# Performance work log

Measured on AMD Instinct MI355X. Metric: run time of the kernel, lower is better.

## Reference

```python
import jax, jax.numpy as jnp
import numpy as np

NUM_QUBITS = 12
ENC_COPIES = 1
ANSATZ_COPIES = 2
BATCH = 1024
NUM_THETAS = NUM_QUBITS * (ANSATZ_COPIES + 1) * 2  # 72

_H = jnp.asarray(np.array([[1.0, 1.0], [1.0, -1.0]], np.complex64) / np.sqrt(2.0))


def _apply_1q(state, U, q):
    # state: [B, 2, 2, ..., 2] (n qubit axes); apply 2x2 unitary U on qubit q
    s = jnp.moveaxis(state, 1 + q, -1)
    s = jnp.einsum('...j,ij->...i', s, U)
    return jnp.moveaxis(s, -1, 1 + q)


def _apply_zpow(state, t, q):
    # cirq Z**t = diag(1, e^{i*pi*t}); t is scalar or per-batch [B]
    n = state.ndim - 1
    phase = jnp.exp(1j * jnp.pi * t).astype(jnp.complex64)
    factor = jnp.stack([jnp.ones_like(phase), phase], axis=-1)
    if factor.ndim == 2:  # batched exponent -> broadcast over other qubit axes
        factor = factor.reshape((factor.shape[0],) + (1,) * (n - 1) + (2,))
    s = jnp.moveaxis(state, 1 + q, -1)
    return jnp.moveaxis(s * factor, -1, 1 + q)


def _ypow_unitary(t):
    # cirq Y**t up to global phase e^{i*pi*t/2} (irrelevant for Z expectations)
    a = 0.5 * jnp.pi * t
    c, s = jnp.cos(a), jnp.sin(a)
    return jnp.stack([jnp.stack([c, -s]), jnp.stack([s, c])]).astype(jnp.complex64)


def _apply_cnot(state, c, t):
    s = jnp.moveaxis(state, (1 + c, 1 + t), (-2, -1))
    s = jnp.stack([s[..., 0, :], s[..., 1, ::-1]], axis=-2)
    return jnp.moveaxis(s, (-2, -1), (1 + c, 1 + t))


def _encoding_block(state, x):
    # FirstOrderPauliZEncoding: per copy, per qubit: H then Z**x_q
    for _ in range(ENC_COPIES):
        for q in range(NUM_QUBITS):
            state = _apply_1q(state, _H, q)
            state = _apply_zpow(state, x[:, q], q)
    return state


def _ansatz_block(state, th, with_cnot):
    # EfficientSU2 layer: Y**th[q,0], Z**th[q,1] per qubit, then CNOT chain
    for q in range(NUM_QUBITS):
        state = _apply_1q(state, _ypow_unitary(th[q, 0]), q)
        state = _apply_zpow(state, th[q, 1], q)
    if with_cnot:
        for q in range(NUM_QUBITS - 1):
            state = _apply_cnot(state, q, q + 1)
    return state


_enc = jax.checkpoint(_encoding_block)
_ans_cnot = jax.checkpoint(lambda st, th: _ansatz_block(st, th, True))
_ans_last = jax.checkpoint(lambda st, th: _ansatz_block(st, th, False))


def _circuit(inputs, thetas):
    b = inputs.shape[0]
    state = jnp.zeros((b, 2 ** NUM_QUBITS), jnp.complex64).at[:, 0].set(1.0)
    state = state.reshape((b,) + (2,) * NUM_QUBITS)
    state = _enc(state, inputs)
    th = thetas.reshape(ANSATZ_COPIES + 1, NUM_QUBITS, 2)
    for l in range(ANSATZ_COPIES + 1):
        state = (_ans_cnot if l < ANSATZ_COPIES else _ans_last)(state, th[l])
    # readouts: <Z_q> for each qubit
    probs = state.real ** 2 + state.imag ** 2
    exps = []
    for q in range(NUM_QUBITS):
        axes = tuple(a for a in range(1, NUM_QUBITS + 1) if a != 1 + q)
        p = probs.sum(axis=axes)  # [B, 2]
        exps.append(p[:, 0] - p[:, 1])
    return jnp.stack(exps, axis=-1)  # [B, NUM_QUBITS]


def setup_inputs() -> dict:
    key = jax.random.key(0)
    k1, k2 = jax.random.split(key)
    inputs = jax.random.uniform(k1, (BATCH, NUM_QUBITS), jnp.float32)
    thetas = jax.random.uniform(k2, (NUM_THETAS,), jnp.float32, minval=-1.0, maxval=1.0)
    return {"inputs": inputs, "thetas": thetas}


def reference(inputs, thetas):
    return _circuit(inputs, thetas)
```

## Files before the change

kernel.cpp:

```cpp
#include <hip/hip_runtime.h>


#define PI_F 3.14159265358979323846f
#define NR 16

typedef __attribute__((ext_vector_type(2))) float v2f;
typedef __attribute__((ext_vector_type(4))) float v4f;

__device__ __forceinline__ v2f mkv(float x, float y) { v2f r; r.x = x; r.y = y; return r; }

__device__ __forceinline__ v2f cmul(v2f a, v2f b) {
    return a.x * b + a.y * mkv(-b.y, b.x);
}
__device__ __forceinline__ v2f cmulc(v2f a, v2f b) {
    return a.x * mkv(b.x, -b.y) + a.y * mkv(b.y, b.x);
}

template<int M>
__device__ __forceinline__ float lane_xor_f(float v) {
    if constexpr (M == 1) {
        return __int_as_float(__builtin_amdgcn_update_dpp(
            0, __float_as_int(v), 0xB1, 0xF, 0xF, false));
    } else if constexpr (M == 2) {
        return __int_as_float(__builtin_amdgcn_update_dpp(
            0, __float_as_int(v), 0x4E, 0xF, 0xF, false));
    } else if constexpr (M == 4) {
        return __int_as_float(__builtin_amdgcn_ds_swizzle(__float_as_int(v), 0x101F));
    } else if constexpr (M == 8) {
        return __int_as_float(__builtin_amdgcn_ds_swizzle(__float_as_int(v), 0x201F));
    } else if constexpr (M == 16) {
        return __int_as_float(__builtin_amdgcn_ds_swizzle(__float_as_int(v), 0x401F));
    } else {
        return __shfl_xor(v, 32, 64);
    }
}
template<int M>
__device__ __forceinline__ v2f lane_xor_v(v2f v) {
    return mkv(lane_xor_f<M>(v.x), lane_xor_f<M>(v.y));
}

template<int RB>
__device__ __forceinline__ void ypow_reg(v2f (&a)[NR], float c, float s) {
    #pragma unroll
    for (int r0 = 0; r0 < NR; ++r0) {
        if ((r0 >> RB) & 1) continue;
        const int r1 = r0 | (1 << RB);
        v2f a0 = a[r0], a1 = a[r1];
        a[r0] = c * a0 - s * a1;
        a[r1] = s * a0 + c * a1;
    }
}

template<int M>
__device__ __forceinline__ void ypow_lane(v2f (&a)[NR], int lane, float c, float s) {
    const float k1 = (lane & M) ? s : -s;
    #pragma unroll
    for (int r = 0; r < NR; ++r) {
        v2f p = lane_xor_v<M>(a[r]);
        a[r] = c * a[r] + k1 * p;
    }
}

__device__ __forceinline__ void ypowB(v2f (&a)[NR], const float* __restrict__ th) {
    { float s,c; __sincosf(0.5f*PI_F*th[16], &s,&c); ypow_reg<3>(a,c,s); }
    { float s,c; __sincosf(0.5f*PI_F*th[18], &s,&c); ypow_reg<2>(a,c,s); }
    { float s,c; __sincosf(0.5f*PI_F*th[20], &s,&c); ypow_reg<1>(a,c,s); }
    { float s,c; __sincosf(0.5f*PI_F*th[22], &s,&c); ypow_reg<0>(a,c,s); }
}

__device__ __forceinline__ void ypow_lanes(v2f (&a)[NR], int lane,
                                           const float* __restrict__ th) {
    { float s,c; __sincosf(0.5f*PI_F*th[4],  &s,&c); ypow_lane<32>(a,lane,c,s); }
    { float s,c; __sincosf(0.5f*PI_F*th[6],  &s,&c); ypow_lane<16>(a,lane,c,s); }
    { float s,c; __sincosf(0.5f*PI_F*th[8],  &s,&c); ypow_lane<8>(a,lane,c,s); }
    { float s,c; __sincosf(0.5f*PI_F*th[10], &s,&c); ypow_lane<4>(a,lane,c,s); }
    { float s,c; __sincosf(0.5f*PI_F*th[12], &s,&c); ypow_lane<2>(a,lane,c,s); }
    { float s,c; __sincosf(0.5f*PI_F*th[14], &s,&c); ypow_lane<1>(a,lane,c,s); }
}

__device__ __forceinline__ void exchange_BB(v2f (&a)[NR], char* bufc,
                                            int w, int lane, bool preSync,
                                            float c0, float s0, float c1, float s1) {
    if (preSync) __syncthreads();
    const int v_ = (w >> 1) & 1;
    const int u_ = v_ ^ (w & 1);
    const int s9 = ((lane >> 5) ^ u_) & 1;
    const int wbyte = (s9 << 14) | ((lane & 31) << 9) | (u_ << 4) | (v_ << 3);
    #pragma unroll
    for (int r = 0; r < NR; ++r) {
        const int byt = wbyte | (r << 5);
        const int key = (((byt >> 9) ^ (byt >> 12)) & 7) << 4;
        *(v2f*)(bufc + (byt ^ key)) = a[r];
    }
    __syncthreads();
    const float ky00 = (w & 2) ? s0 : c0;
    const float ky01 = (w & 2) ? c0 : -s0;
    const float ky10 = (w & 1) ? s1 : c1;
    const float ky11 = (w & 1) ? c1 : -s1;
    const float k00 = ky10*ky00, k01 = ky10*ky01, k10 = ky11*ky00, k11 = ky11*ky01;
    #pragma unroll
    for (int r = 0; r < NR; ++r) {
        const int ylow = (lane << 4) | r;
        const int t = ylow ^ (ylow >> 1);
        const int base = t << 5;
        const int key = (((base >> 9) ^ (base >> 12)) & 7) << 4;
        v4f p01 = *(const v4f*)(bufc + (base ^ key));
        v4f p23 = *(const v4f*)(bufc + ((base | 16) ^ key));
        a[r] = k00 * p01.xy + k01 * p01.zw + k10 * p23.xy + k11 * p23.zw;
        if ((r & 7) == 7) asm volatile("" ::: "memory");
    }
}

__device__ __forceinline__ void fused_z_B(v2f (&a)[NR], int w, int lane,
                                          const float* __restrict__ th) {
    float alpha = ((w & 2) ? th[1] : 0.0f) + ((w & 1) ? th[3] : 0.0f);
    #pragma unroll
    for (int k = 0; k < 6; ++k)
        alpha += ((lane >> k) & 1) ? th[2*(7-k)+1] : 0.0f;
    float zbs, zbc; __sincosf(PI_F * alpha, &zbs, &zbc);
    v2f zq[4];
    #pragma unroll
    for (int j = 0; j < 4; ++j) {
        float ss, cc; __sincosf(PI_F * th[2*(11-j)+1], &ss, &cc);
        zq[j] = mkv(cc, ss);
    }
    v2f cur = mkv(zbc, zbs);
    a[0] = cmul(a[0], cur);
    #pragma unroll
    for (int k = 1; k < NR; ++k) {
        const int bit = __builtin_ctz(k);
        const int g = k ^ (k >> 1);
        cur = ((g >> bit) & 1) ? cmul(cur, zq[bit]) : cmulc(cur, zq[bit]);
        a[g] = cmul(a[g], cur);
    }
}

__global__ __launch_bounds__(256) void vqc_kernel(
    const float* __restrict__ inputs,
    const float* __restrict__ thetas,
    float* __restrict__ out)
{
    __shared__ __align__(16) char bufc[32768];

    const int b = blockIdx.x;
    const int tid = threadIdx.x;
    const int w = tid >> 6;
    const int lane = tid & 63;
    const float* x = inputs + b * 12;

    v2f a[NR];

    float phb = 0.0f;
    #pragma unroll
    for (int k = 0; k < 6; ++k)
        phb += ((lane >> k) & 1) ? x[7 - k] : 0.0f;
    float cbs, cbc; __sincosf(PI_F * phb, &cbs, &cbc);
    v2f cisb = mkv(cbc, cbs);
    float e0s, e0c; __sincosf(PI_F * x[0], &e0s, &e0c);
    float e1s, e1c; __sincosf(PI_F * x[1], &e1s, &e1c);
    float sa, ca; __sincosf(0.5f * PI_F * thetas[0], &sa, &ca);
    float sb, cb; __sincosf(0.5f * PI_F * thetas[2], &sb, &cb);
    v2f F0 = (w & 2) ? mkv(sa + ca*e0c,  ca*e0s)
                     : mkv(ca - sa*e0c, -sa*e0s);
    v2f F1 = (w & 1) ? mkv(sb + cb*e1c,  cb*e1s)
                     : mkv(cb - sb*e1c, -sb*e1s);
    v2f g0 = cmul(cmul(F0, F1), cisb);
    g0 = g0 * 0.015625f;
    v2f zr[4];
    #pragma unroll
    for (int j = 0; j < 4; ++j) {
        float ss, cc; __sincosf(PI_F * x[11 - j], &ss, &cc);
        zr[j] = mkv(cc, ss);
    }
    {
        v2f cur = g0;
        a[0] = cur;
        #pragma unroll
        for (int k = 1; k < NR; ++k) {
            const int bit = __builtin_ctz(k);
            const int g = k ^ (k >> 1);
            cur = ((g >> bit) & 1) ? cmul(cur, zr[bit]) : cmulc(cur, zr[bit]);
            a[g] = cur;
        }
    }

    const float* th0 = thetas;
    const float* th1 = thetas + 24;
    const float* th2 = thetas + 48;

    ypowB(a, th0);
    ypow_lanes(a, lane, th0);
    fused_z_B(a, w, lane, th0);
    { float s0,c0,s1,c1;
      __sincosf(0.5f*PI_F*th1[0], &s0,&c0);
      __sincosf(0.5f*PI_F*th1[2], &s1,&c1);
      exchange_BB(a, bufc, w, lane, false, c0,s0,c1,s1); }

    ypowB(a, th1);
    ypow_lanes(a, lane, th1);
    fused_z_B(a, w, lane, th1);
    { float s0,c0,s1,c1;
      __sincosf(0.5f*PI_F*th2[0], &s0,&c0);
      __sincosf(0.5f*PI_F*th2[2], &s1,&c1);
      exchange_BB(a, bufc, w, lane, true, c0,s0,c1,s1); }

    ypowB(a, th2);
    ypow_lanes(a, lane, th2);

    float totalP = 0.0f;
    float D[4] = {0, 0, 0, 0};
    #pragma unroll
    for (int r = 0; r < NR; ++r) {
        const float p = a[r].x * a[r].x + a[r].y * a[r].y;
        totalP += p;
        #pragma unroll
        for (int j = 0; j < 4; ++j)
            D[j] += ((r >> j) & 1) ? -p : p;
    }
    float* redBuf = (float*)bufc;
    __syncthreads();
    #pragma unroll
    for (int q = 0; q < 12; ++q) {
        float v;
        if (q == 0)      v = (w & 2) ? -totalP : totalP;
        else if (q == 1) v = (w & 1) ? -totalP : totalP;
        else if (q <= 7) v = ((lane >> (7 - q)) & 1) ? -totalP : totalP;
        else             v = D[11 - q];
        v += lane_xor_f<32>(v);
        v += lane_xor_f<16>(v);
        v += lane_xor_f<8>(v);
        v += lane_xor_f<4>(v);
        v += lane_xor_f<2>(v);
        v += lane_xor_f<1>(v);
        if (lane == 0) redBuf[w * 12 + q] = v;
    }
    __syncthreads();
    if (tid < 12)
        out[b * 12 + tid] = redBuf[tid] + redBuf[12 + tid]
                          + redBuf[24 + tid] + redBuf[36 + tid];
}

extern "C" void kernel_launch(void* const* d_in, const int* in_sizes, int n_in,
                              void* d_out, int out_size, void* d_ws, size_t ws_size,
                              hipStream_t stream) {
    const float* inputs = (const float*)d_in[0];
    const float* thetas = (const float*)d_in[1];
    float* out = (float*)d_out;
    vqc_kernel<<<dim3(1024), dim3(256), 0, stream>>>(inputs, thetas, out);
}
```

Measured before the change: 81.94 us.

## Split state over 8 waves with 8 registers per thread and three-qubit exchange

Changes the state distribution from 4 waves x 16 register amplitudes to 8 waves x 8 registers per thread, launching 512 threads per block. The LDS exchange now mixes three wave-held qubits per pass instead of two, with a new swizzle layout, and the xor-16 lane swap switches from ds_swizzle to shfl. This halves per-thread register work and raises the number of active waves, at the cost of more LDS reads per exchange and more cross-wave reduction.

After: 86.27 us. 5.3% more time.

```diff
diff --git a/kernel.cpp b/kernel.cpp
--- a/kernel.cpp
+++ b/kernel.cpp
@@ -2,7 +2,7 @@
 
 
 #define PI_F 3.14159265358979323846f
-#define NR 16
+#define NR 8
 
 typedef __attribute__((ext_vector_type(2))) float v2f;
 typedef __attribute__((ext_vector_type(4))) float v4f;
@@ -29,7 +29,7 @@
     } else if constexpr (M == 8) {
         return __int_as_float(__builtin_amdgcn_ds_swizzle(__float_as_int(v), 0x201F));
     } else if constexpr (M == 16) {
-        return __int_as_float(__builtin_amdgcn_ds_swizzle(__float_as_int(v), 0x401F));
+        return __shfl_xor(v, 16, 64);
     } else {
         return __shfl_xor(v, 32, 64);
     }
@@ -61,8 +61,7 @@
     }
 }
 
-__device__ __forceinline__ void ypowB(v2f (&a)[NR], const float* __restrict__ th) {
-    { float s,c; __sincosf(0.5f*PI_F*th[16], &s,&c); ypow_reg<3>(a,c,s); }
+__device__ __forceinline__ void ypow_regs(v2f (&a)[NR], const float* __restrict__ th) {
     { float s,c; __sincosf(0.5f*PI_F*th[18], &s,&c); ypow_reg<2>(a,c,s); }
     { float s,c; __sincosf(0.5f*PI_F*th[20], &s,&c); ypow_reg<1>(a,c,s); }
     { float s,c; __sincosf(0.5f*PI_F*th[22], &s,&c); ypow_reg<0>(a,c,s); }
@@ -70,57 +69,73 @@
 
 __device__ __forceinline__ void ypow_lanes(v2f (&a)[NR], int lane,
                                            const float* __restrict__ th) {
-    { float s,c; __sincosf(0.5f*PI_F*th[4],  &s,&c); ypow_lane<32>(a,lane,c,s); }
-    { float s,c; __sincosf(0.5f*PI_F*th[6],  &s,&c); ypow_lane<16>(a,lane,c,s); }
-    { float s,c; __sincosf(0.5f*PI_F*th[8],  &s,&c); ypow_lane<8>(a,lane,c,s); }
-    { float s,c; __sincosf(0.5f*PI_F*th[10], &s,&c); ypow_lane<4>(a,lane,c,s); }
-    { float s,c; __sincosf(0.5f*PI_F*th[12], &s,&c); ypow_lane<2>(a,lane,c,s); }
-    { float s,c; __sincosf(0.5f*PI_F*th[14], &s,&c); ypow_lane<1>(a,lane,c,s); }
-}
-
-__device__ __forceinline__ void exchange_BB(v2f (&a)[NR], char* bufc,
-                                            int w, int lane, bool preSync,
-                                            float c0, float s0, float c1, float s1) {
+    { float s,c; __sincosf(0.5f*PI_F*th[6],  &s,&c); ypow_lane<32>(a,lane,c,s); }
+    { float s,c; __sincosf(0.5f*PI_F*th[8],  &s,&c); ypow_lane<16>(a,lane,c,s); }
+    { float s,c; __sincosf(0.5f*PI_F*th[10], &s,&c); ypow_lane<8>(a,lane,c,s); }
+    { float s,c; __sincosf(0.5f*PI_F*th[12], &s,&c); ypow_lane<4>(a,lane,c,s); }
+    { float s,c; __sincosf(0.5f*PI_F*th[14], &s,&c); ypow_lane<2>(a,lane,c,s); }
+    { float s,c; __sincosf(0.5f*PI_F*th[16], &s,&c); ypow_lane<1>(a,lane,c,s); }
+}
+
+__device__ __forceinline__ void exchange_C(v2f (&a)[NR], char* bufc,
+                                           int wv, int lane, bool preSync,
+                                           float c0, float s0, float c1, float s1,
+                                           float c2, float s2) {
     if (preSync) __syncthreads();
-    const int v_ = (w >> 1) & 1;
-    const int u_ = v_ ^ (w & 1);
-    const int s9 = ((lane >> 5) ^ u_) & 1;
-    const int wbyte = (s9 << 14) | ((lane & 31) << 9) | (u_ << 4) | (v_ << 3);
-    #pragma unroll
-    for (int r = 0; r < NR; ++r) {
-        const int byt = wbyte | (r << 5);
-        const int key = (((byt >> 9) ^ (byt >> 12)) & 7) << 4;
-        *(v2f*)(bufc + (byt ^ key)) = a[r];
+    const int z11 = (wv >> 2) & 1;
+    const int z10 = ((wv >> 1) ^ (wv >> 2)) & 1;
+    const int z9  = (wv ^ (wv >> 1) ^ (wv >> 2)) & 1;
+    const int m_w = (z9 << 2) | (z10 << 1) | z11;
+    int U6 = lane; U6 ^= U6 >> 1; U6 ^= U6 >> 2; U6 ^= U6 >> 4; U6 &= 63;
+    if (z9) U6 ^= 63;
+    const int kxW   = (U6 >> 1) & 3;
+    const int key6W = (U6 >> 3) & 1;
+    const int wbase = (U6 << 9) | ((((m_w >> 1) & 3) ^ kxW) << 4) | ((m_w & 1) << 3);
+    const int ymask = (U6 & 1) ? 7 : 0;
+    #pragma unroll
+    for (int r = 0; r < NR; ++r) {
+        const int low3 = ((r ^ (r >> 1) ^ (r >> 2)) & 7) ^ ymask;
+        *(v2f*)(bufc + (wbase | ((low3 ^ key6W) << 6))) = a[r];
     }
     __syncthreads();
-    const float ky00 = (w & 2) ? s0 : c0;
-    const float ky01 = (w & 2) ? c0 : -s0;
-    const float ky10 = (w & 1) ? s1 : c1;
-    const float ky11 = (w & 1) ? c1 : -s1;
-    const float k00 = ky10*ky00, k01 = ky10*ky01, k10 = ky11*ky00, k11 = ky11*ky01;
-    #pragma unroll
-    for (int r = 0; r < NR; ++r) {
-        const int ylow = (lane << 4) | r;
-        const int t = ylow ^ (ylow >> 1);
-        const int base = t << 5;
-        const int key = (((base >> 9) ^ (base >> 12)) & 7) << 4;
-        v4f p01 = *(const v4f*)(bufc + (base ^ key));
-        v4f p23 = *(const v4f*)(bufc + ((base | 16) ^ key));
-        a[r] = k00 * p01.xy + k01 * p01.zw + k10 * p23.xy + k11 * p23.zw;
-        if ((r & 7) == 7) asm volatile("" ::: "memory");
-    }
-}
-
-__device__ __forceinline__ void fused_z_B(v2f (&a)[NR], int w, int lane,
-                                          const float* __restrict__ th) {
-    float alpha = ((w & 2) ? th[1] : 0.0f) + ((w & 1) ? th[3] : 0.0f);
+    const float A0 = (wv & 4) ? s0 : c0, A1 = (wv & 4) ? c0 : -s0;
+    const float B0 = (wv & 2) ? s1 : c1, B1 = (wv & 2) ? c1 : -s1;
+    const float C0 = (wv & 1) ? s2 : c2, C1 = (wv & 1) ? c2 : -s2;
+    float k0[4], k1[4];
+    #pragma unroll
+    for (int c = 0; c < 4; ++c) {
+        const float CB = ((c & 2) ? C1 : C0) * ((c & 1) ? B1 : B0);
+        k0[c] = CB * A0; k1[c] = CB * A1;
+    }
+    const int kxR   = (lane >> 1) & 3;
+    const int key6R = (lane >> 3) & 1;
+    const int rbase = lane << 9;
+    #pragma unroll
+    for (int r = 0; r < NR; ++r) {
+        const int hi = rbase | ((r ^ key6R) << 6);
+        v4f ch0 = *(const v4f*)(bufc + (hi | ((0 ^ kxR) << 4)));
+        v4f ch1 = *(const v4f*)(bufc + (hi | ((1 ^ kxR) << 4)));
+        v4f ch2 = *(const v4f*)(bufc + (hi | ((2 ^ kxR) << 4)));
+        v4f ch3 = *(const v4f*)(bufc + (hi | ((3 ^ kxR) << 4)));
+        a[r] = k0[0]*ch0.xy + k1[0]*ch0.zw
+             + k0[1]*ch1.xy + k1[1]*ch1.zw
+             + k0[2]*ch2.xy + k1[2]*ch2.zw
+             + k0[3]*ch3.xy + k1[3]*ch3.zw;
+        asm volatile("" ::: "memory");
+    }
+}
+
+__device__ __forceinline__ void fused_z(v2f (&a)[NR], int wv, int lane,
+                                        const float* __restrict__ th) {
+    float alpha = ((wv & 4) ? th[1] : 0.0f) + ((wv & 2) ? th[3] : 0.0f)
+                + ((wv & 1) ? th[5] : 0.0f);
     #pragma unroll
     for (int k = 0; k < 6; ++k)
-        alpha += ((lane >> k) & 1) ? th[2*(7-k)+1] : 0.0f;
+        alpha += ((lane >> k) & 1) ? th[2*(8-k)+1] : 0.0f;
     float zbs, zbc; __sincosf(PI_F * alpha, &zbs, &zbc);
-    v2f zq[4];
-    #pragma unroll
-    for (int j = 0; j < 4; ++j) {
+    v2f zq[3];
+    #pragma unroll
+    for (int j = 0; j < 3; ++j) {
         float ss, cc; __sincosf(PI_F * th[2*(11-j)+1], &ss, &cc);
         zq[j] = mkv(cc, ss);
     }
@@ -135,7 +150,7 @@
     }
 }
 
-__global__ __launch_bounds__(256) void vqc_kernel(
+__global__ __launch_bounds__(512) void vqc_kernel(
     const float* __restrict__ inputs,
     const float* __restrict__ thetas,
     float* __restrict__ out)
@@ -144,7 +159,7 @@
 
     const int b = blockIdx.x;
     const int tid = threadIdx.x;
-    const int w = tid >> 6;
+    const int wv = tid >> 6;
     const int lane = tid & 63;
     const float* x = inputs + b * 12;
 
@@ -153,24 +168,25 @@
     float phb = 0.0f;
     #pragma unroll
     for (int k = 0; k < 6; ++k)
-        phb += ((lane >> k) & 1) ? x[7 - k] : 0.0f;
+        phb += ((lane >> k) & 1) ? x[8 - k] : 0.0f;
     float cbs, cbc; __sincosf(PI_F * phb, &cbs, &cbc);
     v2f cisb = mkv(cbc, cbs);
     float e0s, e0c; __sincosf(PI_F * x[0], &e0s, &e0c);
     float e1s, e1c; __sincosf(PI_F * x[1], &e1s, &e1c);
+    float e2s, e2c; __sincosf(PI_F * x[2], &e2s, &e2c);
     float sa, ca; __sincosf(0.5f * PI_F * thetas[0], &sa, &ca);
     float sb, cb; __sincosf(0.5f * PI_F * thetas[2], &sb, &cb);
-    v2f F0 = (w & 2) ? mkv(sa + ca*e0c,  ca*e0s)
-                     : mkv(ca - sa*e0c, -sa*e0s);
-    v2f F1 = (w & 1) ? mkv(sb + cb*e1c,  cb*e1s)
-                     : mkv(cb - sb*e1c, -sb*e1s);
-    v2f g0 = cmul(cmul(F0, F1), cisb);
+    float sc, cc2; __sincosf(0.5f * PI_F * thetas[4], &sc, &cc2);
+    v2f F0 = (wv & 4) ? mkv(sa + ca*e0c,  ca*e0s) : mkv(ca - sa*e0c, -sa*e0s);
+    v2f F1 = (wv & 2) ? mkv(sb + cb*e1c,  cb*e1s) : mkv(cb - sb*e1c, -sb*e1s);
+    v2f F2 = (wv & 1) ? mkv(sc + cc2*e2c, cc2*e2s) : mkv(cc2 - sc*e2c, -sc*e2s);
+    v2f g0 = cmul(cmul(cmul(F0, F1), F2), cisb);
     g0 = g0 * 0.015625f;
-    v2f zr[4];
-    #pragma unroll
-    for (int j = 0; j < 4; ++j) {
-        float ss, cc; __sincosf(PI_F * x[11 - j], &ss, &cc);
-        zr[j] = mkv(cc, ss);
+    v2f zr[3];
+    #pragma unroll
+    for (int j = 0; j < 3; ++j) {
+        float ss, zc; __sincosf(PI_F * x[11 - j], &ss, &zc);
+        zr[j] = mkv(zc, ss);
     }
     {
         v2f cur = g0;
@@ -188,33 +204,35 @@
     const float* th1 = thetas + 24;
     const float* th2 = thetas + 48;
 
-    ypowB(a, th0);
+    ypow_regs(a, th0);
     ypow_lanes(a, lane, th0);
-    fused_z_B(a, w, lane, th0);
-    { float s0,c0,s1,c1;
+    fused_z(a, wv, lane, th0);
+    { float s0,c0,s1,c1,s2,c2;
       __sincosf(0.5f*PI_F*th1[0], &s0,&c0);
       __sincosf(0.5f*PI_F*th1[2], &s1,&c1);
-      exchange_BB(a, bufc, w, lane, false, c0,s0,c1,s1); }
-
-    ypowB(a, th1);
+      __sincosf(0.5f*PI_F*th1[4], &s2,&c2);
+      exchange_C(a, bufc, wv, lane, false, c0,s0,c1,s1,c2,s2); }
+
+    ypow_regs(a, th1);
     ypow_lanes(a, lane, th1);
-    fused_z_B(a, w, lane, th1);
-    { float s0,c0,s1,c1;
+    fused_z(a, wv, lane, th1);
+    { float s0,c0,s1,c1,s2,c2;
       __sincosf(0.5f*PI_F*th2[0], &s0,&c0);
       __sincosf(0.5f*PI_F*th2[2], &s1,&c1);
-      exchange_BB(a, bufc, w, lane, true, c0,s0,c1,s1); }
-
-    ypowB(a, th2);
+      __sincosf(0.5f*PI_F*th2[4], &s2,&c2);
+      exchange_C(a, bufc, wv, lane, true, c0,s0,c1,s1,c2,s2); }
+
+    ypow_regs(a, th2);
     ypow_lanes(a, lane, th2);
 
     float totalP = 0.0f;
-    float D[4] = {0, 0, 0, 0};
+    float D[3] = {0, 0, 0};
     #pragma unroll
     for (int r = 0; r < NR; ++r) {
         const float p = a[r].x * a[r].x + a[r].y * a[r].y;
         totalP += p;
         #pragma unroll
-        for (int j = 0; j < 4; ++j)
+        for (int j = 0; j < 3; ++j)
             D[j] += ((r >> j) & 1) ? -p : p;
     }
     float* redBuf = (float*)bufc;
@@ -222,9 +240,10 @@
     #pragma unroll
     for (int q = 0; q < 12; ++q) {
         float v;
-        if (q == 0)      v = (w & 2) ? -totalP : totalP;
-        else if (q == 1) v = (w & 1) ? -totalP : totalP;
-        else if (q <= 7) v = ((lane >> (7 - q)) & 1) ? -totalP : totalP;
+        if (q == 0)      v = (wv & 4) ? -totalP : totalP;
+        else if (q == 1) v = (wv & 2) ? -totalP : totalP;
+        else if (q == 2) v = (wv & 1) ? -totalP : totalP;
+        else if (q <= 8) v = ((lane >> (8 - q)) & 1) ? -totalP : totalP;
         else             v = D[11 - q];
         v += lane_xor_f<32>(v);
         v += lane_xor_f<16>(v);
@@ -232,12 +251,15 @@
         v += lane_xor_f<4>(v);
         v += lane_xor_f<2>(v);
         v += lane_xor_f<1>(v);
-        if (lane == 0) redBuf[w * 12 + q] = v;
+        if (lane == 0) redBuf[wv * 12 + q] = v;
     }
     __syncthreads();
-    if (tid < 12)
-        out[b * 12 + tid] = redBuf[tid] + redBuf[12 + tid]
-                          + redBuf[24 + tid] + redBuf[36 + tid];
+    if (tid < 12) {
+        float s = 0.0f;
+        #pragma unroll
+        for (int w8 = 0; w8 < 8; ++w8) s += redBuf[w8 * 12 + tid];
+        out[b * 12 + tid] = s;
+    }
 }
 
 extern "C" void kernel_launch(void* const* d_in, const int* in_sizes, int n_in,
@@ -246,5 +268,5 @@
     const float* inputs = (const float*)d_in[0];
     const float* thetas = (const float*)d_in[1];
     float* out = (float*)d_out;
-    vqc_kernel<<<dim3(1024), dim3(256), 0, stream>>>(inputs, thetas, out);
-}
+    vqc_kernel<<<dim3(1024), dim3(512), 0, stream>>>(inputs, thetas, out);
+}
```
